# Performance work log

Hardware: AMD Instinct MI355X
Metric: run time of the kernel (lower is better)

The kernel has to match this reference:

```python
import jax, jax.numpy as jnp
import numpy as np

EPS = 1e-5  # torch LayerNorm default


def _layer_norm(x, gamma, beta):
    mu = jnp.mean(x, axis=-1, keepdims=True)
    var = jnp.mean(jnp.square(x - mu), axis=-1, keepdims=True)
    return (x - mu) * jax.lax.rsqrt(var + EPS) * gamma + beta


def setup_inputs() -> dict:
    key = jax.random.key(0)
    ks = jax.random.split(key, 6)
    B, T, S, A, H = 256, 2048, 39, 4, 256
    D = S + A
    observations = jax.random.normal(ks[0], (B, T, S), dtype=jnp.float32)
    actions = jax.random.normal(ks[1], (B, T, A), dtype=jnp.float32)
    # MLP params (orthogonal gain=0.1 in torch; random scale 0.1 here)
    W1 = jax.random.normal(ks[2], (D, H), dtype=jnp.float32) * 0.1
    b1 = jnp.zeros((H,), dtype=jnp.float32)
    g1 = jnp.ones((H,), dtype=jnp.float32)
    beta1 = jnp.zeros((H,), dtype=jnp.float32)
    W2 = jax.random.normal(ks[3], (H, H), dtype=jnp.float32) * 0.1
    b2 = jnp.zeros((H,), dtype=jnp.float32)
    g2 = jnp.ones((H,), dtype=jnp.float32)
    beta2 = jnp.zeros((H,), dtype=jnp.float32)
    W3 = jax.random.normal(ks[4], (H, 1), dtype=jnp.float32) * 0.1
    b3 = jnp.zeros((1,), dtype=jnp.float32)
    return {"observations": observations, "actions": actions,
            "W1": W1, "b1": b1, "g1": g1, "beta1": beta1,
            "W2": W2, "b2": b2, "g2": g2, "beta2": beta2,
            "W3": W3, "b3": b3}


def reference(observations, actions, W1, b1, g1, beta1, W2, b2, g2, beta2, W3, b3):
    # Batched equivalent of the per-(b,t) loop: concat -> (Linear+LN+ReLU) x2 -> Linear(.,1)
    x = jnp.concatenate([observations, actions], axis=-1)  # [B, T, S+A]
    h = jax.nn.relu(_layer_norm(x @ W1 + b1, g1, beta1))    # [B, T, H]
    h = jax.nn.relu(_layer_norm(h @ W2 + b2, g2, beta2))    # [B, T, H]
    r = (h @ W3 + b3)[..., 0]                                # [B, T] per-step reward
    return jnp.sum(r, axis=-1)                               # [B] segment reward
```

## Files before the change

kernel.cpp:

```cpp
#include <hip/hip_runtime.h>
#include <hip/hip_bf16.h>

typedef __attribute__((ext_vector_type(8)))  short short8;
typedef __attribute__((ext_vector_type(4)))  float f32x4;
typedef __attribute__((ext_vector_type(16))) float f32x16;

__device__ __forceinline__ unsigned short f2bf(float x) {
  __hip_bfloat16 h = __float2bfloat16(x);
  return (unsigned short)__builtin_bit_cast(short, h);
}
__device__ __forceinline__ unsigned packbf2(float lo, float hi2) {
  return (unsigned)f2bf(lo) | ((unsigned)f2bf(hi2) << 16);
}

__global__ void repack_zero(const float* __restrict__ W1, const float* __restrict__ W2,
                            short* __restrict__ Wp, float* __restrict__ out, int outn) {
  int id = blockIdx.x * 256 + threadIdx.x;
  if (blockIdx.x == 0 && threadIdx.x < outn) out[threadIdx.x] = 0.f;
  if (id >= 152 * 64) return;
  int fragidx = id >> 6, lane = id & 63;
  const float* W; int ks, mt, kmax;
  if (fragidx < 24) { W = W1; ks = fragidx >> 3; mt = fragidx & 7; kmax = 43; }
  else { int f2 = fragidx - 24; W = W2; ks = f2 >> 3; mt = f2 & 7; kmax = 256; }
  int h = 32 * mt + (lane & 31);
  int k0 = 16 * ks + 8 * (lane >> 5);
  short8 v;
  #pragma unroll
  for (int i = 0; i < 8; ++i) {
    int k = k0 + i;
    float x = (k < kmax) ? W[(long)k * 256 + h] : 0.f;
    v[i] = (short)f2bf(x);
  }
  *(short8*)(Wp + (long)fragidx * 512 + lane * 8) = v;
}

__device__ __forceinline__ short8 pack8(const float* v) {
  union { unsigned u[4]; short8 s; } c;
  #pragma unroll
  for (int j = 0; j < 4; ++j) c.u[j] = packbf2(v[2 * j], v[2 * j + 1]);
  return c.s;
}

__launch_bounds__(256, 2)
__global__ void srm2(const float* __restrict__ obs, const float* __restrict__ act,
                     const float* __restrict__ b1, const float* __restrict__ g1,
                     const float* __restrict__ be1,
                     const float* __restrict__ b2, const float* __restrict__ g2,
                     const float* __restrict__ be2,
                     const float* __restrict__ W3, const float* __restrict__ b3,
                     const short* __restrict__ Wp, float* __restrict__ out) {
  __shared__ float pb1[256], pg1[256], pe1[256];
  __shared__ float pb2[256], pg2[256], pe2[256], pw3[256];
  const int tid = threadIdx.x;
  pb1[tid] = b1[tid]; pg1[tid] = g1[tid]; pe1[tid] = be1[tid];
  pb2[tid] = b2[tid]; pg2[tid] = g2[tid]; pe2[tid] = be2[tid];
  pw3[tid] = W3[tid];
  const float b3v = b3[0];
  __syncthreads();

  const int wave = tid >> 6, lane = tid & 63;
  const int l31 = lane & 31, hi = lane >> 5;
  const int row0 = blockIdx.x * 128 + wave * 32;
  const int n = row0 + l31;
  const int bidx = row0 >> 11;

  const float* orow = obs + (long)n * 39;
  const float* arow = act + (long)n * 4;
  short8 bx0, bx1, bx2;
  {
    float v[8];
    #pragma unroll
    for (int i = 0; i < 8; ++i) v[i] = orow[8 * hi + i];
    bx0 = pack8(v);
    #pragma unroll
    for (int i = 0; i < 8; ++i) v[i] = orow[16 + 8 * hi + i];
    bx1 = pack8(v);
    #pragma unroll
    for (int i = 0; i < 8; ++i) {
      int k = 32 + 8 * hi + i;
      float t = 0.f;
      if (k < 39) t = orow[k]; else if (k < 43) t = arow[k - 39];
      v[i] = t;
    }
    bx2 = pack8(v);
  }

  const short8* W1v = (const short8*)Wp;
  const short8* W2v = (const short8*)(Wp + 24L * 512);

  f32x16 acc[8];
  #pragma unroll
  for (int mt = 0; mt < 8; ++mt) acc[mt] = (f32x16)0.f;

  #pragma unroll
  for (int ks = 0; ks < 3; ++ks) {
    const short8 bb = (ks == 0) ? bx0 : (ks == 1) ? bx1 : bx2;
    #pragma unroll
    for (int mt = 0; mt < 8; ++mt) {
      short8 a = W1v[(ks * 8 + mt) * 64 + lane];
      acc[mt] = __builtin_amdgcn_mfma_f32_32x32x16_bf16(a, bb, acc[mt], 0, 0, 0);
    }
  }

  float mean1, rstd1;
  {
    float s = 0.f, q = 0.f;
    #pragma unroll
    for (int mt = 0; mt < 8; ++mt)
      #pragma unroll
      for (int qq = 0; qq < 4; ++qq) {
        const f32x4 b4 = *(const f32x4*)&pb1[32 * mt + 8 * qq + 4 * hi];
        #pragma unroll
        for (int e = 0; e < 4; ++e) {
          float t = acc[mt][4 * qq + e] + b4[e];
          acc[mt][4 * qq + e] = t;
          s += t; q += t * t;
        }
      }
    s += __shfl_xor(s, 32); q += __shfl_xor(q, 32);
    mean1 = s * (1.f / 256.f);
    rstd1 = rsqrtf(q * (1.f / 256.f) - mean1 * mean1 + 1e-5f);
  }

  unsigned pk[8][4][2];
  #pragma unroll
  for (int mt = 0; mt < 8; ++mt)
    #pragma unroll
    for (int qq = 0; qq < 4; ++qq) {
      const int h0 = 32 * mt + 8 * qq + 4 * hi;
      const f32x4 g4 = *(const f32x4*)&pg1[h0];
      const f32x4 e4 = *(const f32x4*)&pe1[h0];
      float val[4];
      #pragma unroll
      for (int e = 0; e < 4; ++e) {
        float a = rstd1 * g4[e];
        float c = e4[e] - mean1 * a;
        val[e] = fmaxf(acc[mt][4 * qq + e] * a + c, 0.f);
      }
      pk[mt][qq][0] = packbf2(val[0], val[1]);
      pk[mt][qq][1] = packbf2(val[2], val[3]);
    }

  #pragma unroll
  for (int mt = 0; mt < 8; ++mt) acc[mt] = (f32x16)0.f;

  #pragma unroll
  for (int ks = 0; ks < 16; ++ks) {
    const int msrc = ks >> 1, q0 = 2 * (ks & 1), q1 = q0 + 1;
    unsigned c0 = hi ? pk[msrc][q0][0] : pk[msrc][q1][0];
    unsigned c1 = hi ? pk[msrc][q0][1] : pk[msrc][q1][1];
    unsigned r0 = __shfl_xor(c0, 32), r1 = __shfl_xor(c1, 32);
    unsigned o0 = hi ? pk[msrc][q1][0] : pk[msrc][q0][0];
    unsigned o1 = hi ? pk[msrc][q1][1] : pk[msrc][q0][1];
    union { unsigned u[4]; short8 s; } bb;
    bb.u[0] = hi ? r0 : o0; bb.u[1] = hi ? r1 : o1;
    bb.u[2] = hi ? o0 : r0; bb.u[3] = hi ? o1 : r1;
    #pragma unroll
    for (int mt = 0; mt < 8; ++mt) {
      short8 a = W2v[(ks * 8 + mt) * 64 + lane];
      acc[mt] = __builtin_amdgcn_mfma_f32_32x32x16_bf16(a, bb.s, acc[mt], 0, 0, 0);
    }
  }

  float mean2, rstd2;
  {
    float s = 0.f, q = 0.f;
    #pragma unroll
    for (int mt = 0; mt < 8; ++mt)
      #pragma unroll
      for (int qq = 0; qq < 4; ++qq) {
        const f32x4 b4 = *(const f32x4*)&pb2[32 * mt + 8 * qq + 4 * hi];
        #pragma unroll
        for (int e = 0; e < 4; ++e) {
          float t = acc[mt][4 * qq + e] + b4[e];
          acc[mt][4 * qq + e] = t;
          s += t; q += t * t;
        }
      }
    s += __shfl_xor(s, 32); q += __shfl_xor(q, 32);
    mean2 = s * (1.f / 256.f);
    rstd2 = rsqrtf(q * (1.f / 256.f) - mean2 * mean2 + 1e-5f);
  }

  float p = 0.f;
  #pragma unroll
  for (int mt = 0; mt < 8; ++mt)
    #pragma unroll
    for (int qq = 0; qq < 4; ++qq) {
      const int h0 = 32 * mt + 8 * qq + 4 * hi;
      const f32x4 g4 = *(const f32x4*)&pg2[h0];
      const f32x4 e4 = *(const f32x4*)&pe2[h0];
      const f32x4 w4 = *(const f32x4*)&pw3[h0];
      #pragma unroll
      for (int e = 0; e < 4; ++e) {
        float a = rstd2 * g4[e];
        float c = e4[e] - mean2 * a;
        float val = fmaxf(acc[mt][4 * qq + e] * a + c, 0.f);
        p += val * w4[e];
      }
    }
  p += __shfl_xor(p, 32);
  #pragma unroll
  for (int off = 1; off < 32; off <<= 1) p += __shfl_xor(p, off);
  if (lane == 0) atomicAdd(&out[bidx], p + 32.f * b3v);
}

extern "C" void kernel_launch(void* const* d_in, const int* in_sizes, int n_in,
                              void* d_out, int out_size, void* d_ws, size_t ws_size,
                              hipStream_t stream) {
  const float* obs = (const float*)d_in[0];
  const float* act = (const float*)d_in[1];
  const float* W1  = (const float*)d_in[2];
  const float* b1  = (const float*)d_in[3];
  const float* g1  = (const float*)d_in[4];
  const float* be1 = (const float*)d_in[5];
  const float* W2  = (const float*)d_in[6];
  const float* b2  = (const float*)d_in[7];
  const float* g2  = (const float*)d_in[8];
  const float* be2 = (const float*)d_in[9];
  const float* W3  = (const float*)d_in[10];
  const float* b3  = (const float*)d_in[11];
  float* out = (float*)d_out;

  short* Wp = (short*)d_ws;

  repack_zero<<<38, 256, 0, stream>>>(W1, W2, Wp, out, out_size);

  const int n_rows = 256 * 2048;
  srm2<<<n_rows / 128, 256, 0, stream>>>(obs, act, b1, g1, be1,
                                         b2, g2, be2, W3, b3, Wp, out);
}
```

Measured before the change: 376.2 us.

## Split hidden dim across waves with register-resident weights and LDS-staged activations

```diff
diff --git a/kernel.cpp b/kernel.cpp
--- a/kernel.cpp
+++ b/kernel.cpp
@@ -11,6 +11,12 @@
 }
 __device__ __forceinline__ unsigned packbf2(float lo, float hi2) {
   return (unsigned)f2bf(lo) | ((unsigned)f2bf(hi2) << 16);
+}
+__device__ __forceinline__ short8 pack8(const float* v) {
+  union { unsigned u[4]; short8 s; } c;
+  #pragma unroll
+  for (int j = 0; j < 4; ++j) c.u[j] = packbf2(v[2 * j], v[2 * j + 1]);
+  return c.s;
 }
 
 __global__ void repack_zero(const float* __restrict__ W1, const float* __restrict__ W2,
@@ -34,15 +40,10 @@
   *(short8*)(Wp + (long)fragidx * 512 + lane * 8) = v;
 }
 
-__device__ __forceinline__ short8 pack8(const float* v) {
-  union { unsigned u[4]; short8 s; } c;
-  #pragma unroll
-  for (int j = 0; j < 4; ++j) c.u[j] = packbf2(v[2 * j], v[2 * j + 1]);
-  return c.s;
-}
+#define TILES 8
 
 __launch_bounds__(256, 2)
-__global__ void srm2(const float* __restrict__ obs, const float* __restrict__ act,
+__global__ void srm3(const float* __restrict__ obs, const float* __restrict__ act,
                      const float* __restrict__ b1, const float* __restrict__ g1,
                      const float* __restrict__ be1,
                      const float* __restrict__ b2, const float* __restrict__ g2,
@@ -51,158 +52,179 @@
                      const short* __restrict__ Wp, float* __restrict__ out) {
   __shared__ float pb1[256], pg1[256], pe1[256];
   __shared__ float pb2[256], pg2[256], pe2[256], pw3[256];
+  __shared__ float2 sq1[4][32], sq2[4][32];
+  __shared__ short H1[32 * 256];
+
   const int tid = threadIdx.x;
   pb1[tid] = b1[tid]; pg1[tid] = g1[tid]; pe1[tid] = be1[tid];
   pb2[tid] = b2[tid]; pg2[tid] = g2[tid]; pe2[tid] = be2[tid];
   pw3[tid] = W3[tid];
   const float b3v = b3[0];
-  __syncthreads();
 
   const int wave = tid >> 6, lane = tid & 63;
   const int l31 = lane & 31, hi = lane >> 5;
-  const int row0 = blockIdx.x * 128 + wave * 32;
-  const int n = row0 + l31;
-  const int bidx = row0 >> 11;
-
-  const float* orow = obs + (long)n * 39;
-  const float* arow = act + (long)n * 4;
-  short8 bx0, bx1, bx2;
-  {
-    float v[8];
-    #pragma unroll
-    for (int i = 0; i < 8; ++i) v[i] = orow[8 * hi + i];
-    bx0 = pack8(v);
-    #pragma unroll
-    for (int i = 0; i < 8; ++i) v[i] = orow[16 + 8 * hi + i];
-    bx1 = pack8(v);
-    #pragma unroll
-    for (int i = 0; i < 8; ++i) {
-      int k = 32 + 8 * hi + i;
-      float t = 0.f;
-      if (k < 39) t = orow[k]; else if (k < 43) t = arow[k - 39];
-      v[i] = t;
-    }
-    bx2 = pack8(v);
-  }
+  const int mt0 = 2 * wave;
 
   const short8* W1v = (const short8*)Wp;
   const short8* W2v = (const short8*)(Wp + 24L * 512);
-
-  f32x16 acc[8];
-  #pragma unroll
-  for (int mt = 0; mt < 8; ++mt) acc[mt] = (f32x16)0.f;
-
-  #pragma unroll
-  for (int ks = 0; ks < 3; ++ks) {
-    const short8 bb = (ks == 0) ? bx0 : (ks == 1) ? bx1 : bx2;
-    #pragma unroll
-    for (int mt = 0; mt < 8; ++mt) {
-      short8 a = W1v[(ks * 8 + mt) * 64 + lane];
-      acc[mt] = __builtin_amdgcn_mfma_f32_32x32x16_bf16(a, bb, acc[mt], 0, 0, 0);
-    }
+  short8 w1f[3][2], w2f[16][2];
+  #pragma unroll
+  for (int ks = 0; ks < 3; ++ks)
+    #pragma unroll
+    for (int j = 0; j < 2; ++j)
+      w1f[ks][j] = W1v[(ks * 8 + mt0 + j) * 64 + lane];
+  #pragma unroll
+  for (int ks = 0; ks < 16; ++ks)
+    #pragma unroll
+    for (int j = 0; j < 2; ++j)
+      w2f[ks][j] = W2v[(ks * 8 + mt0 + j) * 64 + lane];
+
+  __syncthreads();
+
+  const int blockRow0 = blockIdx.x * (TILES * 32);
+  const int bidx = blockRow0 >> 11;
+  const int swz = (l31 & 7) << 4;
+  float ptot = 0.f;
+
+  #pragma unroll 1
+  for (int t = 0; t < TILES; ++t) {
+    const long n = blockRow0 + t * 32 + l31;
+
+    const float* orow = obs + n * 39;
+    const float* arow = act + n * 4;
+    short8 bx[3];
+    {
+      float v[8];
+      #pragma unroll
+      for (int i = 0; i < 8; ++i) v[i] = orow[8 * hi + i];
+      bx[0] = pack8(v);
+      #pragma unroll
+      for (int i = 0; i < 8; ++i) v[i] = orow[16 + 8 * hi + i];
+      bx[1] = pack8(v);
+      #pragma unroll
+      for (int i = 0; i < 8; ++i) {
+        int k = 32 + 8 * hi + i;
+        float tv = 0.f;
+        if (k < 39) tv = orow[k]; else if (k < 43) tv = arow[k - 39];
+        v[i] = tv;
+      }
+      bx[2] = pack8(v);
+    }
+
+    f32x16 acc[2];
+    acc[0] = (f32x16)0.f; acc[1] = (f32x16)0.f;
+
+    #pragma unroll
+    for (int ks = 0; ks < 3; ++ks) {
+      acc[0] = __builtin_amdgcn_mfma_f32_32x32x16_bf16(w1f[ks][0], bx[ks], acc[0], 0, 0, 0);
+      acc[1] = __builtin_amdgcn_mfma_f32_32x32x16_bf16(w1f[ks][1], bx[ks], acc[1], 0, 0, 0);
+    }
+
+    float s = 0.f, q = 0.f;
+    #pragma unroll
+    for (int j = 0; j < 2; ++j)
+      #pragma unroll
+      for (int qq = 0; qq < 4; ++qq) {
+        const f32x4 b4 = *(const f32x4*)&pb1[32 * (mt0 + j) + 8 * qq + 4 * hi];
+        #pragma unroll
+        for (int e = 0; e < 4; ++e) {
+          float tv = acc[j][4 * qq + e] + b4[e];
+          acc[j][4 * qq + e] = tv;
+          s += tv; q += tv * tv;
+        }
+      }
+    s += __shfl_xor(s, 32); q += __shfl_xor(q, 32);
+    if (lane < 32) sq1[wave][l31] = make_float2(s, q);
+    __syncthreads();
+    {
+      float2 a0 = sq1[0][l31], a1 = sq1[1][l31], a2 = sq1[2][l31], a3 = sq1[3][l31];
+      s = a0.x + a1.x + a2.x + a3.x;
+      q = a0.y + a1.y + a2.y + a3.y;
+    }
+    float mean = s * (1.f / 256.f);
+    float rstd = rsqrtf(q * (1.f / 256.f) - mean * mean + 1e-5f);
+
+    #pragma unroll
+    for (int j = 0; j < 2; ++j)
+      #pragma unroll
+      for (int qq = 0; qq < 4; ++qq) {
+        const int h0 = 32 * (mt0 + j) + 8 * qq + 4 * hi;
+        const f32x4 g4 = *(const f32x4*)&pg1[h0];
+        const f32x4 e4 = *(const f32x4*)&pe1[h0];
+        float val[4];
+        #pragma unroll
+        for (int e = 0; e < 4; ++e) {
+          float a = rstd * g4[e];
+          float c = e4[e] - mean * a;
+          val[e] = fmaxf(acc[j][4 * qq + e] * a + c, 0.f);
+        }
+        unsigned lo = packbf2(val[0], val[1]);
+        unsigned hiw = packbf2(val[2], val[3]);
+        int byteoff = ((int)l31 * 512 + 2 * h0) ^ swz;
+        *(uint2*)((char*)H1 + byteoff) = make_uint2(lo, hiw);
+      }
+    __syncthreads();
+
+    acc[0] = (f32x16)0.f; acc[1] = (f32x16)0.f;
+    #pragma unroll
+    for (int ks = 0; ks < 16; ++ks) {
+      int byteoff = ((int)l31 * 512 + 32 * ks + 16 * hi) ^ swz;
+      short8 bb = *(const short8*)((const char*)H1 + byteoff);
+      acc[0] = __builtin_amdgcn_mfma_f32_32x32x16_bf16(w2f[ks][0], bb, acc[0], 0, 0, 0);
+      acc[1] = __builtin_amdgcn_mfma_f32_32x32x16_bf16(w2f[ks][1], bb, acc[1], 0, 0, 0);
+    }
+
+    s = 0.f; q = 0.f;
+    #pragma unroll
+    for (int j = 0; j < 2; ++j)
+      #pragma unroll
+      for (int qq = 0; qq < 4; ++qq) {
+        const f32x4 b4 = *(const f32x4*)&pb2[32 * (mt0 + j) + 8 * qq + 4 * hi];
+        #pragma unroll
+        for (int e = 0; e < 4; ++e) {
+          float tv = acc[j][4 * qq + e] + b4[e];
+          acc[j][4 * qq + e] = tv;
+          s += tv; q += tv * tv;
+        }
+      }
+    s += __shfl_xor(s, 32); q += __shfl_xor(q, 32);
+    if (lane < 32) sq2[wave][l31] = make_float2(s, q);
+    __syncthreads();
+    {
+      float2 a0 = sq2[0][l31], a1 = sq2[1][l31], a2 = sq2[2][l31], a3 = sq2[3][l31];
+      s = a0.x + a1.x + a2.x + a3.x;
+      q = a0.y + a1.y + a2.y + a3.y;
+    }
+    float mean2 = s * (1.f / 256.f);
+    float rstd2 = rsqrtf(q * (1.f / 256.f) - mean2 * mean2 + 1e-5f);
+
+    float p = 0.f;
+    #pragma unroll
+    for (int j = 0; j < 2; ++j)
+      #pragma unroll
+      for (int qq = 0; qq < 4; ++qq) {
+        const int h0 = 32 * (mt0 + j) + 8 * qq + 4 * hi;
+        const f32x4 g4 = *(const f32x4*)&pg2[h0];
+        const f32x4 e4 = *(const f32x4*)&pe2[h0];
+        const f32x4 w4 = *(const f32x4*)&pw3[h0];
+        #pragma unroll
+        for (int e = 0; e < 4; ++e) {
+          float a = rstd2 * g4[e];
+          float c = e4[e] - mean2 * a;
+          float val = fmaxf(acc[j][4 * qq + e] * a + c, 0.f);
+          p += val * w4[e];
+        }
+      }
+    ptot += p;
   }
 
-  float mean1, rstd1;
-  {
-    float s = 0.f, q = 0.f;
-    #pragma unroll
-    for (int mt = 0; mt < 8; ++mt)
-      #pragma unroll
-      for (int qq = 0; qq < 4; ++qq) {
-        const f32x4 b4 = *(const f32x4*)&pb1[32 * mt + 8 * qq + 4 * hi];
-        #pragma unroll
-        for (int e = 0; e < 4; ++e) {
-          float t = acc[mt][4 * qq + e] + b4[e];
-          acc[mt][4 * qq + e] = t;
-          s += t; q += t * t;
-        }
-      }
-    s += __shfl_xor(s, 32); q += __shfl_xor(q, 32);
-    mean1 = s * (1.f / 256.f);
-    rstd1 = rsqrtf(q * (1.f / 256.f) - mean1 * mean1 + 1e-5f);
+  ptot += __shfl_xor(ptot, 32);
+  #pragma unroll
+  for (int off = 1; off < 32; off <<= 1) ptot += __shfl_xor(ptot, off);
+  if (lane == 0) {
+    float add = ptot + (wave == 0 ? (float)(TILES * 32) * b3v : 0.f);
+    atomicAdd(&out[bidx], add);
   }
-
-  unsigned pk[8][4][2];
-  #pragma unroll
-  for (int mt = 0; mt < 8; ++mt)
-    #pragma unroll
-    for (int qq = 0; qq < 4; ++qq) {
-      const int h0 = 32 * mt + 8 * qq + 4 * hi;
-      const f32x4 g4 = *(const f32x4*)&pg1[h0];
-      const f32x4 e4 = *(const f32x4*)&pe1[h0];
-      float val[4];
-      #pragma unroll
-      for (int e = 0; e < 4; ++e) {
-        float a = rstd1 * g4[e];
-        float c = e4[e] - mean1 * a;
-        val[e] = fmaxf(acc[mt][4 * qq + e] * a + c, 0.f);
-      }
-      pk[mt][qq][0] = packbf2(val[0], val[1]);
-      pk[mt][qq][1] = packbf2(val[2], val[3]);
-    }
-
-  #pragma unroll
-  for (int mt = 0; mt < 8; ++mt) acc[mt] = (f32x16)0.f;
-
-  #pragma unroll
-  for (int ks = 0; ks < 16; ++ks) {
-    const int msrc = ks >> 1, q0 = 2 * (ks & 1), q1 = q0 + 1;
-    unsigned c0 = hi ? pk[msrc][q0][0] : pk[msrc][q1][0];
-    unsigned c1 = hi ? pk[msrc][q0][1] : pk[msrc][q1][1];
-    unsigned r0 = __shfl_xor(c0, 32), r1 = __shfl_xor(c1, 32);
-    unsigned o0 = hi ? pk[msrc][q1][0] : pk[msrc][q0][0];
-    unsigned o1 = hi ? pk[msrc][q1][1] : pk[msrc][q0][1];
-    union { unsigned u[4]; short8 s; } bb;
-    bb.u[0] = hi ? r0 : o0; bb.u[1] = hi ? r1 : o1;
-    bb.u[2] = hi ? o0 : r0; bb.u[3] = hi ? o1 : r1;
-    #pragma unroll
-    for (int mt = 0; mt < 8; ++mt) {
-      short8 a = W2v[(ks * 8 + mt) * 64 + lane];
-      acc[mt] = __builtin_amdgcn_mfma_f32_32x32x16_bf16(a, bb.s, acc[mt], 0, 0, 0);
-    }
-  }
-
-  float mean2, rstd2;
-  {
-    float s = 0.f, q = 0.f;
-    #pragma unroll
-    for (int mt = 0; mt < 8; ++mt)
-      #pragma unroll
-      for (int qq = 0; qq < 4; ++qq) {
-        const f32x4 b4 = *(const f32x4*)&pb2[32 * mt + 8 * qq + 4 * hi];
-        #pragma unroll
-        for (int e = 0; e < 4; ++e) {
-          float t = acc[mt][4 * qq + e] + b4[e];
-          acc[mt][4 * qq + e] = t;
-          s += t; q += t * t;
-        }
-      }
-    s += __shfl_xor(s, 32); q += __shfl_xor(q, 32);
-    mean2 = s * (1.f / 256.f);
-    rstd2 = rsqrtf(q * (1.f / 256.f) - mean2 * mean2 + 1e-5f);
-  }
-
-  float p = 0.f;
-  #pragma unroll
-  for (int mt = 0; mt < 8; ++mt)
-    #pragma unroll
-    for (int qq = 0; qq < 4; ++qq) {
-      const int h0 = 32 * mt + 8 * qq + 4 * hi;
-      const f32x4 g4 = *(const f32x4*)&pg2[h0];
-      const f32x4 e4 = *(const f32x4*)&pe2[h0];
-      const f32x4 w4 = *(const f32x4*)&pw3[h0];
-      #pragma unroll
-      for (int e = 0; e < 4; ++e) {
-        float a = rstd2 * g4[e];
-        float c = e4[e] - mean2 * a;
-        float val = fmaxf(acc[mt][4 * qq + e] * a + c, 0.f);
-        p += val * w4[e];
-      }
-    }
-  p += __shfl_xor(p, 32);
-  #pragma unroll
-  for (int off = 1; off < 32; off <<= 1) p += __shfl_xor(p, off);
-  if (lane == 0) atomicAdd(&out[bidx], p + 32.f * b3v);
 }
 
 extern "C" void kernel_launch(void* const* d_in, const int* in_sizes, int n_in,
@@ -227,6 +249,7 @@
   repack_zero<<<38, 256, 0, stream>>>(W1, W2, Wp, out, out_size);
 
   const int n_rows = 256 * 2048;
-  srm2<<<n_rows / 128, 256, 0, stream>>>(obs, act, b1, g1, be1,
-                                         b2, g2, be2, W3, b3, Wp, out);
-}
+  const int n_blocks = n_rows / (TILES * 32);
+  srm3<<<n_blocks, 256, 0, stream>>>(obs, act, b1, g1, be1,
+                                     b2, g2, be2, W3, b3, Wp, out);
+}
```

Result: faster. 348.5 us (-7.4%).
